# Kernel optimization log

Hardware: AMD Instinct MI355X
Metric: run time of the kernel (lower is better)

## Reference

```python
import jax, jax.numpy as jnp
import numpy as np

K = 16  # hardcoded in the torch module (reshape([-1, 16]))


def setup_inputs() -> dict:
    key = jax.random.key(0)
    B, M = 32, 2048
    N = B * M
    ks = jax.random.split(key, 7)
    pos = jax.random.normal(ks[0], (N, 3), dtype=jnp.float32)
    batch = jnp.repeat(jnp.arange(B, dtype=jnp.int32), M)  # sorted, equal-size graphs

    def lin(k_, fi, fo):
        lim = 1.0 / np.sqrt(fi)
        w = jax.random.uniform(k_, (fi, fo), jnp.float32, -lim, lim)
        b = jax.random.uniform(jax.random.fold_in(k_, 1), (fo,), jnp.float32, -lim, lim)
        return w, b

    W1, b1 = lin(ks[1], K * 6, 1024)
    W2, b2 = lin(ks[2], 1024, 256)
    W3, b3 = lin(ks[3], 256, 9)
    return {"pos": pos, "batch": batch, "num_graphs": B,
            "W1": W1, "b1": b1, "W2": W2, "b2": b2, "W3": W3, "b3": b3}


def _knn_idx(pos, num_graphs):
    # equal-size graphs laid out contiguously -> batched brute-force knn
    N = pos.shape[0]
    M = N // num_graphs
    p = pos.reshape(num_graphs, M, 3)
    sq = jnp.sum(p * p, axis=-1)                      # [B, M]
    # squared distances [B, M, M]; self-distance ~0 so loop=True self-edge is kept
    d2 = sq[:, :, None] + sq[:, None, :] - 2.0 * jnp.einsum('bid,bjd->bij', p, p)
    _, idx = jax.lax.top_k(-d2, K)                    # [B, M, K] local indices
    offs = (jnp.arange(num_graphs, dtype=idx.dtype) * M)[:, None, None]
    return (idx + offs).reshape(N, K)                 # global neighbour indices


def reference(pos, batch, num_graphs, W1, b1, W2, b2, W3, b3):
    N = pos.shape[0]
    M = N // num_graphs
    nbr_idx = _knn_idx(pos, num_graphs)               # [N, K]
    neighbours = pos[nbr_idx]                         # [N, K, 3] gather
    center = pos[:, None, :]                          # [N, 1, 3]
    feat = jnp.concatenate(
        [jnp.broadcast_to(center, (N, K, 3)), center - neighbours], axis=2
    ).reshape(N, K * 6)                               # [N, 96]
    h = jax.nn.relu(feat @ W1 + b1)
    h = jax.nn.relu(h @ W2 + b2)
    x9 = h @ W3 + b3                                  # [N, 9]
    pooled = x9.reshape(num_graphs, M, 9).mean(axis=1)  # global_mean_pool -> [B, 9]
    T = pooled[batch].reshape(N, 3, 3)                # gather back per node
    return jnp.einsum('nd,ndk->nk', pos, T)           # bmm([N,1,3],[N,3,3]) squeezed
```

## Files before the change

kernel.cpp:

```cpp
#include <hip/hip_runtime.h>
#include <stdint.h>

#define NPTS   65536
#define MPTS   2048
#define NGRAPH 32

typedef short s16x8 __attribute__((ext_vector_type(8)));
typedef float f32x4 __attribute__((ext_vector_type(4)));

#define FEATP_OFF 0u
#define W1P_OFF   12582912u
#define W2P_OFF   12779520u
#define SACC_OFF  13303808u
#define ZKEY_OFF  13337728u

#define PAD  128
#define ZN   (MPTS + 2 * PAD)

__device__ __forceinline__ unsigned short f2bf(float f) {
  unsigned u = __float_as_uint(f);
  u = (u + 0x7FFFu + ((u >> 16) & 1u)) >> 16;
  return (unsigned short)u;
}

__device__ __forceinline__ void ce32(unsigned& a, unsigned& b) {
  unsigned lo = __builtin_elementwise_min(a, b);
  b = __builtin_elementwise_max(a, b);
  a = lo;
}

template <int N>
__device__ __forceinline__ void sortN(unsigned* k) {
#pragma unroll
  for (int p = 1; p < N; p <<= 1)
#pragma unroll
    for (int q = p; q >= 1; q >>= 1)
#pragma unroll
      for (int j = q % p; j + q < N; j += 2 * q)
#pragma unroll
        for (int i = 0; i < q; ++i)
          if (i + j + q < N)
            if ((i + j) / (2 * p) == (i + j + q) / (2 * p))
              ce32(k[i + j], k[i + j + q]);
}

__device__ __forceinline__ void mergelow8(unsigned r[8], const unsigned b[8]) {
#pragma unroll
  for (int i = 0; i < 8; ++i)
    r[i] = __builtin_elementwise_min(r[i], b[7 - i]);
#pragma unroll
  for (int d = 4; d >= 1; d >>= 1)
#pragma unroll
    for (int i = 0; i < 8; ++i)
      if ((i & d) == 0) ce32(r[i], r[i + d]);
}

__device__ __forceinline__ void mergelow16(unsigned r[16], const unsigned b[16]) {
#pragma unroll
  for (int i = 0; i < 16; ++i)
    r[i] = __builtin_elementwise_min(r[i], b[15 - i]);
#pragma unroll
  for (int d = 8; d >= 1; d >>= 1)
#pragma unroll
    for (int i = 0; i < 16; ++i)
      if ((i & d) == 0) ce32(r[i], r[i + d]);
}

__global__ __launch_bounds__(512) void prep(
    const float* __restrict__ pos, const float* __restrict__ W1,
    const float* __restrict__ W2, unsigned* __restrict__ zkeysG,
    unsigned short* __restrict__ w1p, unsigned short* __restrict__ w2p,
    float* __restrict__ sacc)
{
  __shared__ unsigned sk[MPTS];
  int b = blockIdx.x;
  int tid = threadIdx.x;
  if (b < NGRAPH) {
    const float* gp = pos + (size_t)b * MPTS * 3;
    int w = tid >> 6, l = tid & 63;
    unsigned v[4];
#pragma unroll
    for (int s = 0; s < 4; ++s) {
      int i = w * 256 + s * 64 + l;
      unsigned u = __float_as_uint(gp[i * 3 + 2]);
      u ^= ((unsigned)(((int)u) >> 31)) | 0x80000000u;
      v[s] = (u & 0xFFFFF800u) | (unsigned)i;
    }
#pragma unroll
    for (int kk = 1; kk <= 11; ++kk) {
      const int k2 = 1 << kk;
      if (k2 >= 512) {
        __syncthreads();
#pragma unroll
        for (int s = 0; s < 4; ++s) sk[w * 256 + s * 64 + l] = v[s];
#pragma unroll
        for (int j = k2 >> 1; j >= 256; j >>= 1) {
          __syncthreads();
#pragma unroll
          for (int e = 0; e < 4; ++e) {
            int i = tid + (e << 9);
            int ix = i ^ j;
            if (ix > i) {
              unsigned a = sk[i], b2 = sk[ix];
              bool up = ((i & k2) == 0);
              unsigned lo = __builtin_elementwise_min(a, b2);
              unsigned hi = __builtin_elementwise_max(a, b2);
              sk[i] = up ? lo : hi;
              sk[ix] = up ? hi : lo;
            }
          }
        }
        __syncthreads();
#pragma unroll
        for (int s = 0; s < 4; ++s) v[s] = sk[w * 256 + s * 64 + l];
      }
#pragma unroll
      for (int j = 128; j >= 64; j >>= 1) {
        if (k2 > j) {
          int sd = j >> 6;
#pragma unroll
          for (int s = 0; s < 4; ++s) {
            int sp = s ^ sd;
            if (sp > s) {
              bool up = (((w * 256 + s * 64 + l) & k2) == 0);
              unsigned lo = __builtin_elementwise_min(v[s], v[sp]);
              unsigned hi = __builtin_elementwise_max(v[s], v[sp]);
              v[s] = up ? lo : hi;
              v[sp] = up ? hi : lo;
            }
          }
        }
      }
#pragma unroll
      for (int j = 32; j >= 1; j >>= 1) {
        if (k2 > j) {
#pragma unroll
          for (int s = 0; s < 4; ++s) {
            unsigned p = __shfl_xor(v[s], j, 64);
            bool up = (((w * 256 + s * 64 + l) & k2) == 0);
            bool lower = ((l & j) == 0);
            v[s] = (lower == up) ? __builtin_elementwise_min(v[s], p)
                                 : __builtin_elementwise_max(v[s], p);
          }
        }
      }
    }
#pragma unroll
    for (int s = 0; s < 4; ++s)
      zkeysG[(b << 11) + w * 256 + s * 64 + l] = v[s];
  } else {
    int pid = (b - NGRAPH) * 512 + tid;
    if (pid < 98304) {
      int k = pid >> 10, n = pid & 1023;
      int kt = k >> 5, h = (k >> 3) & 3, j = k & 7;
      int nt = n >> 4, cc = n & 15;
      w1p[((size_t)(kt * 64 + nt) * 64 + h * 16 + cc) * 8 + j] = f2bf(W1[pid]);
    } else if (pid < 98304 + 262144) {
      int t = pid - 98304;
      int k = t >> 8, n = t & 255;
      int kt = k >> 5, h = (k >> 3) & 3, j = k & 7;
      int nt = n >> 4, cc = n & 15;
      w2p[((size_t)(kt * 16 + nt) * 64 + h * 16 + cc) * 8 + j] = f2bf(W2[t]);
    } else if (pid < 360448 + 8192) {
      sacc[pid - 360448] = 0.0f;
    }
  }
}

__global__ __launch_bounds__(512, 4) void knn_feat(
    const float* __restrict__ pos, const unsigned* __restrict__ zkeysG,
    unsigned short* __restrict__ featp)
{
  __shared__ float4 zq[ZN];
  const float INF = __uint_as_float(0x7F800000u);
  int g = blockIdx.x >> 5;
  const float* gp = pos + (size_t)g * MPTS * 3;
  for (int i = threadIdx.x; i < ZN; i += 512) {
    float4 v;
    if (i < PAD) v = make_float4(INF, INF, -INF, INF);
    else if (i >= MPTS + PAD) v = make_float4(INF, INF, INF, INF);
    else {
      int o = (int)(zkeysG[(g << 11) + (i - PAD)] & 0x7FFu);
      float x = gp[o * 3], y = gp[o * 3 + 1], z = gp[o * 3 + 2];
      v = make_float4(x, y, z, fmaf(x, x, fmaf(y, y, z * z)));
    }
    zq[i] = v;
  }
  __syncthreads();

  int l = threadIdx.x & 63, w = threadIdx.x >> 6;
  int qv = l & 7, t = l >> 3;
  int R0 = ((w << 5) | (blockIdx.x & 31)) << 3;
  int R = R0 + qv;
  float4 c = zq[R + PAD];
  float cs = c.w, cz = c.z;
  float zc = 0.5f * (zq[R0 + PAD].z + zq[R0 + PAD + 7].z);

  unsigned run[8];
#pragma unroll
  for (int i = 0; i < 8; ++i) run[i] = 0xFFFFFFFFu;
  unsigned B = 0xFFFFFFFFu;

  int LO = R0 + PAD, HI = R0 + PAD;
  float zl = zq[LO - 1].z, zr = zq[HI].z;

  for (int step = 0; step < 18; ++step) {
    bool canL = (LO >= PAD), canR = (HI + PAD <= ZN);
    unsigned thr = (B > 0xFFFEFFFFu) ? 0xFFFFFFFFu : B + 0x10000u;
    float dl = cz - zl, dr = zr - cz;
    bool doneL = !canL || ((__float_as_uint(dl * dl) & 0xFFFFF800u) > thr);
    bool doneR = !canR || ((__float_as_uint(dr * dr) & 0xFFFFF800u) > thr);
    if (__all(doneL && doneR)) break;

    bool goR = canR && (!canL || ((zr - zc) <= (zc - zl)));
    int base = goR ? HI : LO - PAD;
    if (goR) HI += PAD; else LO -= PAD;

    zl = (LO >= 1) ? zq[LO - 1].z : -INF;
    zr = (HI < ZN) ? zq[HI].z : INF;

    int bt = base + t;
    unsigned k[16];
#pragma unroll
    for (int i = 0; i < 16; ++i) {
      int p = bt + (i << 3);
      float4 P = zq[p];
      float dot = fmaf(c.x, P.x, fmaf(c.y, P.y, c.z * P.z));
      float d2 = fmaf(-2.0f, dot, cs + P.w);
      k[i] = (__float_as_uint(d2) & 0xFFFFF800u) |
             ((unsigned)(p - PAD) & 0x7FFu);
    }
    sortN<8>(k); sortN<8>(k + 8);
    mergelow8(k, k + 8);
    mergelow8(run, k);

    unsigned bb = run[1];
    bb = __builtin_elementwise_max(bb, (unsigned)__shfl_xor(bb, 8, 64));
    bb = __builtin_elementwise_max(bb, (unsigned)__shfl_xor(bb, 16, 64));
    bb = __builtin_elementwise_max(bb, (unsigned)__shfl_xor(bb, 32, 64));
    B = bb;
  }

  unsigned t16[16];
  {
    unsigned oth[8];
#pragma unroll
    for (int i = 0; i < 8; ++i) oth[i] = __shfl_xor(run[i], 8, 64);
#pragma unroll
    for (int i = 0; i < 8; ++i) {
      unsigned a = run[i], x = oth[7 - i];
      t16[i]     = __builtin_elementwise_min(a, x);
      t16[i + 8] = __builtin_elementwise_max(a, x);
    }
#pragma unroll
    for (int d = 4; d >= 1; d >>= 1)
#pragma unroll
      for (int i = 0; i < 16; ++i)
        if ((i & d) == 0) ce32(t16[i], t16[i + d]);
  }
#pragma unroll
  for (int m = 16; m <= 32; m <<= 1) {
    unsigned o2[16];
#pragma unroll
    for (int i = 0; i < 16; ++i) o2[i] = __shfl_xor(t16[i], m, 64);
    mergelow16(t16, o2);
  }

  if (t == 0) {
    float nx[16], ny[16], nz[16];
#pragma unroll
    for (int i = 0; i < 16; ++i) {
      int rk = (int)(t16[i] & 0x7FFu);
      float4 p = zq[rk + PAD];
      nx[i] = p.x; ny[i] = p.y; nz[i] = p.z;
    }
    int n = g * MPTS + R;
    unsigned short* op = featp + (size_t)(n >> 4) * 1536 + (size_t)(n & 15) * 8;
#pragma unroll
    for (int kt = 0; kt < 3; ++kt) {
#pragma unroll
      for (int h = 0; h < 4; ++h) {
        s16x8 v;
#pragma unroll
        for (int j = 0; j < 8; ++j) {
          int f = kt * 32 + h * 8 + j;
          int kn = f / 6, comp = f % 6;
          float val;
          if      (comp == 0) val = c.x;
          else if (comp == 1) val = c.y;
          else if (comp == 2) val = c.z;
          else if (comp == 3) val = c.x - nx[kn];
          else if (comp == 4) val = c.y - ny[kn];
          else                val = c.z - nz[kn];
          v[j] = (short)f2bf(val);
        }
        *(s16x8*)(op + kt * 512 + h * 128) = v;
      }
    }
  }
}

__device__ __forceinline__ void load_b1(s16x8 (&dst)[3],
    const unsigned short* __restrict__ w1p, int nt, int lane) {
#pragma unroll
  for (int kt = 0; kt < 3; ++kt)
    dst[kt] = *(const s16x8*)(w1p + ((size_t)(kt * 64 + nt) * 64 + lane) * 8);
}

__device__ __forceinline__ void load_b2(s16x8 (&dst)[8],
    const unsigned short* __restrict__ w2p, int c, int w, int lane) {
#pragma unroll
  for (int kt2 = 0; kt2 < 4; ++kt2)
#pragma unroll
    for (int j = 0; j < 2; ++j)
      dst[kt2 * 2 + j] = *(const s16x8*)(
          w2p + ((size_t)((c * 4 + kt2) * 16 + (w * 2 + j)) * 64 + lane) * 8);
}

__device__ __forceinline__ void gemm1_step(const s16x8 (&a1)[4][3],
    const s16x8 (&b1f)[3], float bias1,
    unsigned short (*h1buf)[136], int w, int cl, int ks) {
#pragma unroll
  for (int m = 0; m < 4; ++m) {
    f32x4 acc1 = (f32x4){0, 0, 0, 0};
#pragma unroll
    for (int kt = 0; kt < 3; ++kt)
      acc1 = __builtin_amdgcn_mfma_f32_16x16x32_bf16(a1[m][kt], b1f[kt], acc1, 0, 0, 0);
#pragma unroll
    for (int r = 0; r < 4; ++r) {
      float v = acc1[r] + bias1;
      v = v > 0.0f ? v : 0.0f;
      h1buf[m * 16 + ks * 4 + r][w * 16 + cl] = f2bf(v);
    }
  }
}

__device__ __forceinline__ void gemm2_step(const s16x8 (&b2f)[8],
    f32x4 (&acc2)[4][2], const unsigned short (*h1buf)[136], int cl, int ks) {
#pragma unroll
  for (int kt2 = 0; kt2 < 4; ++kt2) {
    s16x8 afr[4];
#pragma unroll
    for (int m = 0; m < 4; ++m)
      afr[m] = *(const s16x8*)&h1buf[m * 16 + cl][kt2 * 32 + ks * 8];
#pragma unroll
    for (int j = 0; j < 2; ++j)
#pragma unroll
      for (int m = 0; m < 4; ++m)
        acc2[m][j] = __builtin_amdgcn_mfma_f32_16x16x32_bf16(
            afr[m], b2f[kt2 * 2 + j], acc2[m][j], 0, 0, 0);
  }
}

__global__ __launch_bounds__(512, 2) void mlp_fused(
    const unsigned short* __restrict__ featp,
    const unsigned short* __restrict__ w1p,
    const unsigned short* __restrict__ w2p,
    const float* __restrict__ b1, const float* __restrict__ b2,
    float* __restrict__ sacc)
{
  __shared__ unsigned short h1c[2][64][136];

  int tid = threadIdx.x;
  int w = tid >> 6, lane = tid & 63;
  int b = blockIdx.x;
  int g = b >> 5;
  int ks = lane >> 4;
  int cl = lane & 15;

  s16x8 a1[4][3];
#pragma unroll
  for (int m = 0; m < 4; ++m) {
    const unsigned short* ap = featp + (size_t)(b * 4 + m) * 1536 + (size_t)lane * 8;
#pragma unroll
    for (int kt = 0; kt < 3; ++kt) a1[m][kt] = *(const s16x8*)(ap + kt * 512);
  }

  f32x4 acc2[4][2];
#pragma unroll
  for (int m = 0; m < 4; ++m) {
    acc2[m][0] = (f32x4){0, 0, 0, 0};
    acc2[m][1] = (f32x4){0, 0, 0, 0};
  }

  float bias1v[8];
#pragma unroll
  for (int c = 0; c < 8; ++c) bias1v[c] = b1[(c * 8 + w) * 16 + cl];

  s16x8 b1f[3];
  load_b1(b1f, w1p, w, lane);
  s16x8 b2a[8], b2b[8];
  load_b2(b2a, w2p, 0, w, lane);

#pragma unroll
  for (int cc = 0; cc < 8; cc += 2) {
    gemm1_step(a1, b1f, bias1v[cc], h1c[0], w, cl, ks);
    load_b1(b1f, w1p, (cc + 1) * 8 + w, lane);
    __syncthreads();
    load_b2(b2b, w2p, cc + 1, w, lane);
    gemm2_step(b2a, acc2, h1c[0], cl, ks);

    gemm1_step(a1, b1f, bias1v[cc + 1], h1c[1], w, cl, ks);
    if (cc + 2 < 8) load_b1(b1f, w1p, (cc + 2) * 8 + w, lane);
    __syncthreads();
    if (cc + 2 < 8) load_b2(b2a, w2p, cc + 2, w, lane);
    gemm2_step(b2b, acc2, h1c[1], cl, ks);
  }

  float sj0 = 0.0f, sj1 = 0.0f;
  {
    float bias20 = b2[(2 * w + 0) * 16 + cl];
    float bias21 = b2[(2 * w + 1) * 16 + cl];
#pragma unroll
    for (int m = 0; m < 4; ++m)
#pragma unroll
      for (int r = 0; r < 4; ++r) {
        float v0 = acc2[m][0][r] + bias20;
        float v1 = acc2[m][1][r] + bias21;
        sj0 += v0 > 0.0f ? v0 : 0.0f;
        sj1 += v1 > 0.0f ? v1 : 0.0f;
      }
  }
#pragma unroll
  for (int m = 16; m <= 32; m <<= 1) {
    sj0 += __shfl_xor(sj0, m, 64);
    sj1 += __shfl_xor(sj1, m, 64);
  }
  if (ks == 0) {
    atomicAdd(&sacc[g * 256 + (2 * w + 0) * 16 + cl], sj0);
    atomicAdd(&sacc[g * 256 + (2 * w + 1) * 16 + cl], sj1);
  }
}

__global__ __launch_bounds__(256) void finalize(
    const float* __restrict__ pos, const float* __restrict__ sacc,
    const float* __restrict__ W3, const float* __restrict__ b3,
    float* __restrict__ out)
{
  __shared__ float P[9];
  int b = blockIdx.x;
  int g = b >> 3;
  int tid = threadIdx.x;
  if (tid < 9) {
    float acc = 0.0f;
    const float* sp = sacc + g * 256;
#pragma unroll 8
    for (int k = 0; k < 256; ++k) acc = fmaf(sp[k], W3[k * 9 + tid], acc);
    P[tid] = fmaf(acc, 1.0f / (float)MPTS, b3[tid]);
  }
  __syncthreads();
  int n = b * 256 + tid;
  float px = pos[n * 3], py = pos[n * 3 + 1], pz = pos[n * 3 + 2];
#pragma unroll
  for (int k2 = 0; k2 < 3; ++k2)
    out[n * 3 + k2] = fmaf(px, P[k2], fmaf(py, P[3 + k2], pz * P[6 + k2]));
}

extern "C" void kernel_launch(void* const* d_in, const int* in_sizes, int n_in,
                              void* d_out, int out_size, void* d_ws, size_t ws_size,
                              hipStream_t stream) {
  const float* pos  = (const float*)d_in[0];
  const float* W1 = (const float*)d_in[3];
  const float* b1 = (const float*)d_in[4];
  const float* W2 = (const float*)d_in[5];
  const float* b2 = (const float*)d_in[6];
  const float* W3 = (const float*)d_in[7];
  const float* b3 = (const float*)d_in[8];

  char* ws = (char*)d_ws;
  unsigned short* featp = (unsigned short*)(ws + FEATP_OFF);
  unsigned short* w1p   = (unsigned short*)(ws + W1P_OFF);
  unsigned short* w2p   = (unsigned short*)(ws + W2P_OFF);
  float*          sacc  = (float*)(ws + SACC_OFF);
  unsigned*       zkeysG = (unsigned*)(ws + ZKEY_OFF);
  float*          out = (float*)d_out;

  prep<<<dim3(752), dim3(512), 0, stream>>>(pos, W1, W2, zkeysG, w1p, w2p, sacc);
  knn_feat<<<dim3(1024), dim3(512), 0, stream>>>(pos, zkeysG, featp);
  mlp_fused<<<dim3(1024), dim3(512), 0, stream>>>(featp, w1p, w2p, b1, b2, sacc);
  finalize<<<dim3(256), dim3(256), 0, stream>>>(pos, sacc, W3, b3, out);
}
```

Before: 125.8 us.

## Double MLP row tile per block and stage features in LDS

The fused MLP kernel now handles 128 rows per block instead of 64 and runs half as many blocks. Feature tiles are staged once into shared memory, and each W1/W2 fragment load is reused across 8 row tiles, halving weight traffic per row. The old double-buffered software pipeline for h1 is replaced by a single buffer with two barriers per chunk, and occupancy is raised to 3 blocks per CU. The kNN search bounds are also tightened to the real point range so it no longer walks into the padding.

```diff
diff --git a/kernel.cpp b/kernel.cpp
--- a/kernel.cpp
+++ b/kernel.cpp
@@ -205,7 +205,7 @@
   float zl = zq[LO - 1].z, zr = zq[HI].z;
 
   for (int step = 0; step < 18; ++step) {
-    bool canL = (LO >= PAD), canR = (HI + PAD <= ZN);
+    bool canL = (LO > PAD), canR = (HI < MPTS + PAD);
     unsigned thr = (B > 0xFFFEFFFFu) ? 0xFFFFFFFFu : B + 0x10000u;
     float dl = cz - zl, dr = zr - cz;
     bool doneL = !canL || ((__float_as_uint(dl * dl) & 0xFFFFF800u) > thr);
@@ -317,68 +317,35 @@
           w2p + ((size_t)((c * 4 + kt2) * 16 + (w * 2 + j)) * 64 + lane) * 8);
 }
 
-__device__ __forceinline__ void gemm1_step(const s16x8 (&a1)[4][3],
-    const s16x8 (&b1f)[3], float bias1,
-    unsigned short (*h1buf)[136], int w, int cl, int ks) {
-#pragma unroll
-  for (int m = 0; m < 4; ++m) {
-    f32x4 acc1 = (f32x4){0, 0, 0, 0};
-#pragma unroll
-    for (int kt = 0; kt < 3; ++kt)
-      acc1 = __builtin_amdgcn_mfma_f32_16x16x32_bf16(a1[m][kt], b1f[kt], acc1, 0, 0, 0);
-#pragma unroll
-    for (int r = 0; r < 4; ++r) {
-      float v = acc1[r] + bias1;
-      v = v > 0.0f ? v : 0.0f;
-      h1buf[m * 16 + ks * 4 + r][w * 16 + cl] = f2bf(v);
-    }
-  }
-}
-
-__device__ __forceinline__ void gemm2_step(const s16x8 (&b2f)[8],
-    f32x4 (&acc2)[4][2], const unsigned short (*h1buf)[136], int cl, int ks) {
-#pragma unroll
-  for (int kt2 = 0; kt2 < 4; ++kt2) {
-    s16x8 afr[4];
-#pragma unroll
-    for (int m = 0; m < 4; ++m)
-      afr[m] = *(const s16x8*)&h1buf[m * 16 + cl][kt2 * 32 + ks * 8];
-#pragma unroll
-    for (int j = 0; j < 2; ++j)
-#pragma unroll
-      for (int m = 0; m < 4; ++m)
-        acc2[m][j] = __builtin_amdgcn_mfma_f32_16x16x32_bf16(
-            afr[m], b2f[kt2 * 2 + j], acc2[m][j], 0, 0, 0);
-  }
-}
-
-__global__ __launch_bounds__(512, 2) void mlp_fused(
+__global__ __launch_bounds__(512, 3) void mlp_fused(
     const unsigned short* __restrict__ featp,
     const unsigned short* __restrict__ w1p,
     const unsigned short* __restrict__ w2p,
     const float* __restrict__ b1, const float* __restrict__ b2,
     float* __restrict__ sacc)
 {
-  __shared__ unsigned short h1c[2][64][136];
+  __shared__ unsigned short h1c[128][136];
+  __shared__ unsigned short featL[12288];
 
   int tid = threadIdx.x;
   int w = tid >> 6, lane = tid & 63;
   int b = blockIdx.x;
-  int g = b >> 5;
+  int g = b >> 4;
   int ks = lane >> 4;
   int cl = lane & 15;
 
-  s16x8 a1[4][3];
-#pragma unroll
-  for (int m = 0; m < 4; ++m) {
-    const unsigned short* ap = featp + (size_t)(b * 4 + m) * 1536 + (size_t)lane * 8;
-#pragma unroll
-    for (int kt = 0; kt < 3; ++kt) a1[m][kt] = *(const s16x8*)(ap + kt * 512);
-  }
-
-  f32x4 acc2[4][2];
-#pragma unroll
-  for (int m = 0; m < 4; ++m) {
+  {
+    const unsigned short* fp = featp + (size_t)b * 12288;
+#pragma unroll
+    for (int e = 0; e < 3; ++e) {
+      int i = (e * 512 + tid) * 8;
+      *(s16x8*)&featL[i] = *(const s16x8*)&fp[i];
+    }
+  }
+
+  f32x4 acc2[8][2];
+#pragma unroll
+  for (int m = 0; m < 8; ++m) {
     acc2[m][0] = (f32x4){0, 0, 0, 0};
     acc2[m][1] = (f32x4){0, 0, 0, 0};
   }
@@ -387,24 +354,48 @@
 #pragma unroll
   for (int c = 0; c < 8; ++c) bias1v[c] = b1[(c * 8 + w) * 16 + cl];
 
-  s16x8 b1f[3];
-  load_b1(b1f, w1p, w, lane);
-  s16x8 b2a[8], b2b[8];
-  load_b2(b2a, w2p, 0, w, lane);
-
-#pragma unroll
-  for (int cc = 0; cc < 8; cc += 2) {
-    gemm1_step(a1, b1f, bias1v[cc], h1c[0], w, cl, ks);
-    load_b1(b1f, w1p, (cc + 1) * 8 + w, lane);
+  __syncthreads();
+
+  for (int c = 0; c < 8; ++c) {
+    s16x8 b2f[8];
+    load_b2(b2f, w2p, c, w, lane);
+
+    s16x8 b1f[3];
+    load_b1(b1f, w1p, c * 8 + w, lane);
+    float bias1 = bias1v[c];
+#pragma unroll
+    for (int m = 0; m < 8; ++m) {
+      s16x8 af[3];
+#pragma unroll
+      for (int kt = 0; kt < 3; ++kt)
+        af[kt] = *(const s16x8*)&featL[m * 1536 + kt * 512 + lane * 8];
+      f32x4 acc1 = (f32x4){0, 0, 0, 0};
+#pragma unroll
+      for (int kt = 0; kt < 3; ++kt)
+        acc1 = __builtin_amdgcn_mfma_f32_16x16x32_bf16(af[kt], b1f[kt], acc1, 0, 0, 0);
+#pragma unroll
+      for (int r = 0; r < 4; ++r) {
+        float v = acc1[r] + bias1;
+        v = v > 0.0f ? v : 0.0f;
+        h1c[m * 16 + ks * 4 + r][w * 16 + cl] = f2bf(v);
+      }
+    }
     __syncthreads();
-    load_b2(b2b, w2p, cc + 1, w, lane);
-    gemm2_step(b2a, acc2, h1c[0], cl, ks);
-
-    gemm1_step(a1, b1f, bias1v[cc + 1], h1c[1], w, cl, ks);
-    if (cc + 2 < 8) load_b1(b1f, w1p, (cc + 2) * 8 + w, lane);
+
+#pragma unroll
+    for (int kt2 = 0; kt2 < 4; ++kt2) {
+      s16x8 afr[8];
+#pragma unroll
+      for (int m = 0; m < 8; ++m)
+        afr[m] = *(const s16x8*)&h1c[m * 16 + cl][kt2 * 32 + ks * 8];
+#pragma unroll
+      for (int j = 0; j < 2; ++j)
+#pragma unroll
+        for (int m = 0; m < 8; ++m)
+          acc2[m][j] = __builtin_amdgcn_mfma_f32_16x16x32_bf16(
+              afr[m], b2f[kt2 * 2 + j], acc2[m][j], 0, 0, 0);
+    }
     __syncthreads();
-    if (cc + 2 < 8) load_b2(b2a, w2p, cc + 2, w, lane);
-    gemm2_step(b2b, acc2, h1c[1], cl, ks);
   }
 
   float sj0 = 0.0f, sj1 = 0.0f;
@@ -412,7 +403,7 @@
     float bias20 = b2[(2 * w + 0) * 16 + cl];
     float bias21 = b2[(2 * w + 1) * 16 + cl];
 #pragma unroll
-    for (int m = 0; m < 4; ++m)
+    for (int m = 0; m < 8; ++m)
 #pragma unroll
       for (int r = 0; r < 4; ++r) {
         float v0 = acc2[m][0][r] + bias20;
@@ -477,6 +468,6 @@
 
   prep<<<dim3(752), dim3(512), 0, stream>>>(pos, W1, W2, zkeysG, w1p, w2p, sacc);
   knn_feat<<<dim3(1024), dim3(512), 0, stream>>>(pos, zkeysG, featp);
-  mlp_fused<<<dim3(1024), dim3(512), 0, stream>>>(featp, w1p, w2p, b1, b2, sacc);
+  mlp_fused<<<dim3(512), dim3(512), 0, stream>>>(featp, w1p, w2p, b1, b2, sacc);
   finalize<<<dim3(256), dim3(256), 0, stream>>>(pos, sacc, W3, b3, out);
 }
```

New measurement: 127.7 us. About the same (+1.5%).
